# Optimization experiments

Hardware: AMD Instinct MI355X
Metric: run time of the kernel (lower is better)

Reference implementation:

```python
import jax, jax.numpy as jnp
import numpy as np

D_MODEL = 768
N_HEADS = 12
D_HEAD = D_MODEL // N_HEADS
B, S = 2, 2048


def setup_inputs() -> dict:
    key = jax.random.key(0)
    k1, k2, k3, k4, k5 = jax.random.split(key, 5)
    scale_in = 1.0 / np.sqrt(D_MODEL)
    return {
        "x": jax.random.normal(k1, (B, S, D_MODEL), dtype=jnp.float32),
        "W_qkv": jax.random.normal(k2, (3 * D_MODEL, D_MODEL), dtype=jnp.float32) * scale_in,
        "b_qkv": jax.random.normal(k3, (3 * D_MODEL,), dtype=jnp.float32) * 0.01,
        "W_o": jax.random.normal(k4, (D_MODEL, D_MODEL), dtype=jnp.float32) * scale_in,
        "b_o": jax.random.normal(k5, (D_MODEL,), dtype=jnp.float32) * 0.01,
    }


def reference(x, W_qkv, b_qkv, W_o, b_o):
    b, s, d = x.shape
    # QKV projection (torch Linear: x @ W^T + b), then split into q, k, v
    qkv = x @ W_qkv.T + b_qkv                      # [b, s, 3d]
    q, k, v = jnp.split(qkv, 3, axis=-1)           # each [b, s, d]
    # reshape to heads: [b, h, s, d_head]
    def to_heads(t):
        return t.reshape(b, s, N_HEADS, D_HEAD).transpose(0, 2, 1, 3)
    q, k, v = to_heads(q), to_heads(k), to_heads(v)
    # full attention scores with causal mask
    scores = jnp.einsum("bhqd,bhkd->bhqk", q, k) * (D_HEAD ** -0.5)
    causal = jnp.tril(jnp.ones((s, s), dtype=bool))
    scores = jnp.where(causal, scores, -jnp.inf)
    probas = jax.nn.softmax(scores, axis=-1)
    z = jnp.einsum("bhqk,bhkd->bhqd", probas, v)   # [b, h, s, d_head]
    z = z.transpose(0, 2, 1, 3).reshape(b, s, d)
    return z @ W_o.T + b_o
```

## Files before the change

### kernel.cpp

```cpp
#include <hip/hip_runtime.h>
#include <hip/hip_bf16.h>
#include <stdint.h>

#define D_MODEL 768
#define N_HEADS 12
#define D_HEAD  64
#define BATCH   2
#define SEQ     2048
#define M_TOTAL (BATCH*SEQ)
#define N_QKV   (3*D_MODEL)

typedef float  floatx4 __attribute__((ext_vector_type(4)));
typedef short  shortx8 __attribute__((ext_vector_type(8)));

#if __has_builtin(__builtin_amdgcn_exp2f)
#define EXP2(x) __builtin_amdgcn_exp2f(x)
#else
#define EXP2(x) exp2f(x)
#endif

#define Q_SCALE 0.18033688011112042f

static __device__ __forceinline__ unsigned short f2bf(float f) {
  __hip_bfloat16 h = __float2bfloat16(f);
  return *reinterpret_cast<unsigned short*>(&h);
}

static __device__ __forceinline__ void gload_lds16(const void* g, void* l) {
  auto gp = reinterpret_cast<const uint32_t __attribute__((address_space(1)))*>(
      reinterpret_cast<uintptr_t>(g));
  auto lp = reinterpret_cast<uint32_t __attribute__((address_space(3)))*>(
      reinterpret_cast<uintptr_t>(l));
  __builtin_amdgcn_global_load_lds(gp, lp, 16, 0, 0);
}

__global__ void convert_bf16_kernel(const float* __restrict__ x,
                                    const float* __restrict__ wqkv,
                                    const float* __restrict__ wo,
                                    unsigned short* __restrict__ xb,
                                    unsigned short* __restrict__ wqkvb,
                                    unsigned short* __restrict__ wob) {
  const int NX = M_TOTAL * D_MODEL / 4;
  const int NW = N_QKV * D_MODEL / 4;
  const int NO = D_MODEL * D_MODEL / 4;
  const int total = NX + NW + NO;
  for (int i = blockIdx.x * blockDim.x + threadIdx.x; i < total;
       i += gridDim.x * blockDim.x) {
    const float4* src; unsigned short* dst; int j;
    if (i < NX)            { src = (const float4*)x;    dst = xb;    j = i; }
    else if (i < NX + NW)  { src = (const float4*)wqkv; dst = wqkvb; j = i - NX; }
    else                   { src = (const float4*)wo;   dst = wob;   j = i - NX - NW; }
    float4 v = src[j];
    ushort4 o;
    o.x = f2bf(v.x); o.y = f2bf(v.y); o.z = f2bf(v.z); o.w = f2bf(v.w);
    *(ushort4*)(dst + (size_t)j * 4) = o;
  }
}

__launch_bounds__(256, 3)
__global__ void qkv_gemm_kernel(const unsigned short* __restrict__ Xb,
                                const unsigned short* __restrict__ Wb,
                                const float* __restrict__ bias,
                                unsigned short* __restrict__ Qb,
                                unsigned short* __restrict__ Kb,
                                unsigned short* __restrict__ Vt) {
  __shared__ unsigned short Asub[128 * 32];
  __shared__ unsigned short Bsub[128 * 32];
  const int tid  = threadIdx.x;
  const int wave = tid >> 6;
  const int lane = tid & 63;
  const int flat = blockIdx.x;
  const int swz  = (flat & 7) * 72 + (flat >> 3);
  const int m0 = (swz / 18) * 128;
  const int n0 = (swz % 18) * 128;
  const int wm = (wave >> 1) * 64;
  const int wn = (wave & 1) * 64;
  const int srow = lane >> 2;
  const int scol = (lane & 3) * 8;
  const int col  = lane & 15;
  const int grp  = lane >> 4;
  floatx4 acc[4][4] = {};
  for (int kt = 0; kt < D_MODEL; kt += 32) {
    #pragma unroll
    for (int i = 0; i < 2; ++i) {
      int c = wave * 2 + i;
      int row = c * 16 + srow;
      gload_lds16(Xb + (size_t)(m0 + row) * D_MODEL + kt + scol, &Asub[c * 512]);
      gload_lds16(Wb + (size_t)(n0 + row) * D_MODEL + kt + scol, &Bsub[c * 512]);
    }
    __syncthreads();
    shortx8 af[4], bf[4];
    #pragma unroll
    for (int t = 0; t < 4; ++t) {
      af[t] = *(const shortx8*)&Asub[(wm + t * 16 + col) * 32 + grp * 8];
      bf[t] = *(const shortx8*)&Bsub[(wn + t * 16 + col) * 32 + grp * 8];
    }
    #pragma unroll
    for (int i = 0; i < 4; ++i)
      #pragma unroll
      for (int j = 0; j < 4; ++j)
        acc[i][j] = __builtin_amdgcn_mfma_f32_16x16x32_bf16(af[i], bf[j], acc[i][j], 0, 0, 0);
    __syncthreads();
  }
  #pragma unroll
  for (int i = 0; i < 4; ++i) {
    int mbase = m0 + wm + i * 16 + grp * 4;
    int b = mbase >> 11;
    int s = mbase & 2047;
    #pragma unroll
    for (int j = 0; j < 4; ++j) {
      int n   = n0 + wn + j * 16 + col;
      int sel = n / D_MODEL;
      int c   = n % D_MODEL;
      int h   = c >> 6, d = c & 63;
      int bh  = b * N_HEADS + h;
      float bv = bias[n];
      if (sel == 0) {
        #pragma unroll
        for (int r = 0; r < 4; ++r)
          Qb[((size_t)bh * SEQ + s + r) * D_HEAD + d] = f2bf((acc[i][j][r] + bv) * Q_SCALE);
      } else if (sel == 1) {
        #pragma unroll
        for (int r = 0; r < 4; ++r)
          Kb[((size_t)bh * SEQ + s + r) * D_HEAD + d] = f2bf(acc[i][j][r] + bv);
      } else {
        ushort4 o;
        o.x = f2bf(acc[i][j][0] + bv);
        o.y = f2bf(acc[i][j][1] + bv);
        o.z = f2bf(acc[i][j][2] + bv);
        o.w = f2bf(acc[i][j][3] + bv);
        *(ushort4*)&Vt[((size_t)bh * D_HEAD + d) * SEQ + s] = o;
      }
    }
  }
}

__launch_bounds__(256, 3)
__global__ void attn_kernel(const unsigned short* __restrict__ Qb,
                            const unsigned short* __restrict__ Kb,
                            const unsigned short* __restrict__ Vt,
                            unsigned short* __restrict__ Zb) {
  __shared__ unsigned short K_lds[2][64 * 64];
  __shared__ unsigned short V_lds[2][64 * 64];
  __shared__ unsigned short pw[4][16 * 136];
  const int tid  = threadIdx.x;
  const int w    = tid >> 6;
  const int lane = tid & 63;
  const int col  = lane & 15;
  const int grp  = lane >> 4;

  const int i  = blockIdx.x;
  const int v  = (i & 7) * 96 + (i >> 3);
  const int bh = v >> 5;
  const int qb = 31 - (v & 31);
  const int q0 = qb * 64;
  const int qgb = q0 + w * 16;
  const int ntiles = qb + 1;

  const unsigned short* Qrow = Qb + ((size_t)bh * SEQ + qgb + col) * D_HEAD;
  const shortx8 qf0 = *(const shortx8*)(Qrow + grp * 8);
  const shortx8 qf1 = *(const shortx8*)(Qrow + 32 + grp * 8);

  const size_t kbase = (size_t)bh * SEQ * D_HEAD;
  const size_t vbase = (size_t)bh * D_HEAD * SEQ;

  floatx4 acc[4] = {};
  float mrun = -1e30f, lrun = 0.f;
  unsigned short* pwv = pw[w];

#define STAGE(buf, kv0) do {                                                   \
    const size_t kg = kbase + (size_t)(kv0) * D_HEAD;                          \
    _Pragma("unroll")                                                          \
    for (int s_ = 0; s_ < 2; ++s_) {                                           \
      int L_ = w * 2048 + s_ * 1024 + lane * 16;                               \
      int g_ = L_ ^ (((L_ >> 7) & 7) << 4);                                    \
      gload_lds16(Kb + kg + (g_ >> 1), &K_lds[buf][w * 1024 + s_ * 512]);      \
      int row_ = g_ >> 7, cb_ = g_ & 127;                                      \
      gload_lds16(Vt + vbase + (size_t)row_ * SEQ + (kv0) + (cb_ >> 1),        \
                  &V_lds[buf][w * 1024 + s_ * 512]);                           \
    }                                                                          \
  } while (0)

  STAGE(0, 0);
  __syncthreads();

  for (int t = 0; t < ntiles; ++t) {
    const int cur = t & 1;
    const int kv0 = t * 64;
    if (t + 1 < ntiles) STAGE(cur ^ 1, (t + 1) * 64);

    floatx4 st[4];
    #pragma unroll
    for (int nt = 0; nt < 4; ++nt) {
      int r0 = (nt * 16 + col) * 64;
      int sw = (col & 7) << 3;
      shortx8 kf0 = *(const shortx8*)&K_lds[cur][(r0 + grp * 8) ^ sw];
      shortx8 kf1 = *(const shortx8*)&K_lds[cur][(r0 + 32 + grp * 8) ^ sw];
      floatx4 s = {};
      s = __builtin_amdgcn_mfma_f32_16x16x32_bf16(kf0, qf0, s, 0, 0, 0);
      s = __builtin_amdgcn_mfma_f32_16x16x32_bf16(kf1, qf1, s, 0, 0, 0);
      st[nt] = s;
    }
    float tmax = -1e30f;
    if (t == ntiles - 1) {
      const int q = qgb + col;
      #pragma unroll
      for (int nt = 0; nt < 4; ++nt)
        #pragma unroll
        for (int r = 0; r < 4; ++r) {
          int kv = kv0 + nt * 16 + grp * 4 + r;
          float sv = (kv <= q) ? st[nt][r] : -1e30f;
          st[nt][r] = sv;
          tmax = fmaxf(tmax, sv);
        }
    } else {
      #pragma unroll
      for (int nt = 0; nt < 4; ++nt)
        #pragma unroll
        for (int r = 0; r < 4; ++r) tmax = fmaxf(tmax, st[nt][r]);
    }
    tmax = fmaxf(tmax, __shfl_xor(tmax, 16));
    tmax = fmaxf(tmax, __shfl_xor(tmax, 32));
    const float mnew  = fmaxf(mrun, tmax);
    const float alpha = EXP2(mrun - mnew);
    mrun = mnew;
    float rs = 0.f;
    #pragma unroll
    for (int nt = 0; nt < 4; ++nt)
      #pragma unroll
      for (int r = 0; r < 4; ++r) {
        float pv = EXP2(st[nt][r] - mnew);
        st[nt][r] = pv;
        rs += pv;
      }
    rs += __shfl_xor(rs, 16);
    rs += __shfl_xor(rs, 32);
    lrun = lrun * alpha + rs;
    #pragma unroll
    for (int r = 0; r < 4; ++r) {
      float ar = __shfl(alpha, grp * 4 + r);
      #pragma unroll
      for (int dn = 0; dn < 4; ++dn) acc[dn][r] *= ar;
    }
    #pragma unroll
    for (int nt = 0; nt < 4; ++nt) {
      ushort4 po;
      po.x = f2bf(st[nt][0]); po.y = f2bf(st[nt][1]);
      po.z = f2bf(st[nt][2]); po.w = f2bf(st[nt][3]);
      *(ushort4*)&pwv[col * 136 + nt * 16 + grp * 4] = po;
    }
    #pragma unroll
    for (int m = 0; m < 2; ++m) {
      shortx8 pf = *(const shortx8*)&pwv[col * 136 + m * 32 + grp * 8];
      #pragma unroll
      for (int dn = 0; dn < 4; ++dn) {
        int vr = (dn * 16 + col) * 64;
        shortx8 vf = *(const shortx8*)&V_lds[cur][(vr + m * 32 + grp * 8) ^ ((col & 7) << 3)];
        acc[dn] = __builtin_amdgcn_mfma_f32_16x16x32_bf16(pf, vf, acc[dn], 0, 0, 0);
      }
    }
    __syncthreads();
  }
#undef STAGE

  const int b = bh / N_HEADS, h = bh % N_HEADS;
  #pragma unroll
  for (int r = 0; r < 4; ++r) {
    float lr = __shfl(lrun, grp * 4 + r);
    float li = 1.0f / lr;
    int q = qgb + grp * 4 + r;
    #pragma unroll
    for (int dn = 0; dn < 4; ++dn)
      Zb[((size_t)b * SEQ + q) * D_MODEL + h * 64 + dn * 16 + col] = f2bf(acc[dn][r] * li);
  }
}

__launch_bounds__(256, 4)
__global__ void out_gemm_kernel(const unsigned short* __restrict__ Zb,
                                const unsigned short* __restrict__ Wob,
                                const float* __restrict__ bo,
                                float* __restrict__ Out) {
  __shared__ unsigned short Asub[128 * 32];
  __shared__ unsigned short Bsub[64 * 32];
  const int tid  = threadIdx.x;
  const int wave = tid >> 6;
  const int lane = tid & 63;
  const int flat = blockIdx.x;
  const int swz  = (flat & 7) * 48 + (flat >> 3);
  const int m0 = (swz / 12) * 128;
  const int n0 = (swz % 12) * 64;
  const int wm = (wave >> 1) * 64;
  const int wn = (wave & 1) * 32;
  const int srow = lane >> 2;
  const int scol = (lane & 3) * 8;
  const int col  = lane & 15;
  const int grp  = lane >> 4;
  floatx4 acc[4][2] = {};
  for (int kt = 0; kt < D_MODEL; kt += 32) {
    #pragma unroll
    for (int i = 0; i < 2; ++i) {
      int g = wave * 2 + i;
      gload_lds16(Zb + (size_t)(m0 + g * 16 + srow) * D_MODEL + kt + scol, &Asub[g * 512]);
    }
    gload_lds16(Wob + (size_t)(n0 + wave * 16 + srow) * D_MODEL + kt + scol, &Bsub[wave * 512]);
    __syncthreads();
    shortx8 af[4], bf[2];
    #pragma unroll
    for (int t = 0; t < 4; ++t)
      af[t] = *(const shortx8*)&Asub[(wm + t * 16 + col) * 32 + grp * 8];
    #pragma unroll
    for (int u = 0; u < 2; ++u)
      bf[u] = *(const shortx8*)&Bsub[(wn + u * 16 + col) * 32 + grp * 8];
    #pragma unroll
    for (int i = 0; i < 4; ++i)
      #pragma unroll
      for (int jj = 0; jj < 2; ++jj)
        acc[i][jj] = __builtin_amdgcn_mfma_f32_16x16x32_bf16(af[i], bf[jj], acc[i][jj], 0, 0, 0);
    __syncthreads();
  }
  #pragma unroll
  for (int i = 0; i < 4; ++i) {
    int mbase = m0 + wm + i * 16 + grp * 4;
    #pragma unroll
    for (int jj = 0; jj < 2; ++jj) {
      int n = n0 + wn + jj * 16 + col;
      float bv = bo[n];
      #pragma unroll
      for (int r = 0; r < 4; ++r)
        Out[(size_t)(mbase + r) * D_MODEL + n] = acc[i][jj][r] + bv;
    }
  }
}

extern "C" void kernel_launch(void* const* d_in, const int* in_sizes, int n_in,
                              void* d_out, int out_size, void* d_ws, size_t ws_size,
                              hipStream_t stream) {
  const float* x    = (const float*)d_in[0];
  const float* Wqkv = (const float*)d_in[1];
  const float* bqkv = (const float*)d_in[2];
  const float* Wo   = (const float*)d_in[3];
  const float* bo   = (const float*)d_in[4];
  float* out = (float*)d_out;

  unsigned short* ws = (unsigned short*)d_ws;
  const size_t SZ_X   = (size_t)M_TOTAL * D_MODEL;
  const size_t SZ_WQ  = (size_t)N_QKV * D_MODEL;
  const size_t SZ_WO  = (size_t)D_MODEL * D_MODEL;
  unsigned short* Xb    = ws;
  unsigned short* Wqkvb = Xb + SZ_X;
  unsigned short* Wob   = Wqkvb + SZ_WQ;
  unsigned short* Qb    = Wob + SZ_WO;
  unsigned short* Kb    = Qb + SZ_X;
  unsigned short* Vt    = Kb + SZ_X;
  unsigned short* Zb    = Vt + SZ_X;

  convert_bf16_kernel<<<dim3(1024), dim3(256), 0, stream>>>(x, Wqkv, Wo, Xb, Wqkvb, Wob);
  qkv_gemm_kernel<<<dim3(8 * 72), dim3(256), 0, stream>>>(
      Xb, Wqkvb, bqkv, Qb, Kb, Vt);
  attn_kernel<<<dim3(8 * 96), dim3(256), 0, stream>>>(Qb, Kb, Vt, Zb);
  out_gemm_kernel<<<dim3(8 * 48), dim3(256), 0, stream>>>(
      Zb, Wob, bo, out);
}
```

Measured before the change: 170.5 us.

## Double-buffer GEMM LDS tiles and pair causal query blocks in attention

Both GEMM kernels now use double-buffered LDS tiles. The next K-slice is prefetched while MFMAs run on the current one, and only one barrier is needed per iteration. The attention kernel launches half as many blocks, and each block handles a short query tile (p) and its complementary long one (31-p). This evens out the causal work per block, so the tail of imbalanced blocks should shrink. The cost is doubled LDS in the GEMMs, which could lower occupancy. With only 384 attention blocks there may also be too little parallelism to fill the CUs.

```diff
diff --git a/kernel.cpp b/kernel.cpp
--- a/kernel.cpp
+++ b/kernel.cpp
@@ -64,8 +64,8 @@
                                 unsigned short* __restrict__ Qb,
                                 unsigned short* __restrict__ Kb,
                                 unsigned short* __restrict__ Vt) {
-  __shared__ unsigned short Asub[128 * 32];
-  __shared__ unsigned short Bsub[128 * 32];
+  __shared__ unsigned short Asub[2][128 * 32];
+  __shared__ unsigned short Bsub[2][128 * 32];
   const int tid  = threadIdx.x;
   const int wave = tid >> 6;
   const int lane = tid & 63;
@@ -80,20 +80,29 @@
   const int col  = lane & 15;
   const int grp  = lane >> 4;
   floatx4 acc[4][4] = {};
+
+#define QSTAGE(buf, kt) do {                                                     \
+    _Pragma("unroll")                                                            \
+    for (int i_ = 0; i_ < 2; ++i_) {                                             \
+      int c_ = wave * 2 + i_;                                                    \
+      int row_ = c_ * 16 + srow;                                                 \
+      gload_lds16(Xb + (size_t)(m0 + row_) * D_MODEL + (kt) + scol,              \
+                  &Asub[buf][c_ * 512]);                                         \
+      gload_lds16(Wb + (size_t)(n0 + row_) * D_MODEL + (kt) + scol,              \
+                  &Bsub[buf][c_ * 512]);                                         \
+    }                                                                            \
+  } while (0)
+
+  QSTAGE(0, 0);
+  __syncthreads();
   for (int kt = 0; kt < D_MODEL; kt += 32) {
-    #pragma unroll
-    for (int i = 0; i < 2; ++i) {
-      int c = wave * 2 + i;
-      int row = c * 16 + srow;
-      gload_lds16(Xb + (size_t)(m0 + row) * D_MODEL + kt + scol, &Asub[c * 512]);
-      gload_lds16(Wb + (size_t)(n0 + row) * D_MODEL + kt + scol, &Bsub[c * 512]);
-    }
-    __syncthreads();
+    const int cur = (kt >> 5) & 1;
+    if (kt + 32 < D_MODEL) QSTAGE(cur ^ 1, kt + 32);
     shortx8 af[4], bf[4];
     #pragma unroll
     for (int t = 0; t < 4; ++t) {
-      af[t] = *(const shortx8*)&Asub[(wm + t * 16 + col) * 32 + grp * 8];
-      bf[t] = *(const shortx8*)&Bsub[(wn + t * 16 + col) * 32 + grp * 8];
+      af[t] = *(const shortx8*)&Asub[cur][(wm + t * 16 + col) * 32 + grp * 8];
+      bf[t] = *(const shortx8*)&Bsub[cur][(wn + t * 16 + col) * 32 + grp * 8];
     }
     #pragma unroll
     for (int i = 0; i < 4; ++i)
@@ -102,6 +111,8 @@
         acc[i][j] = __builtin_amdgcn_mfma_f32_16x16x32_bf16(af[i], bf[j], acc[i][j], 0, 0, 0);
     __syncthreads();
   }
+#undef QSTAGE
+
   #pragma unroll
   for (int i = 0; i < 4; ++i) {
     int mbase = m0 + wm + i * 16 + grp * 4;
@@ -150,22 +161,13 @@
   const int grp  = lane >> 4;
 
   const int i  = blockIdx.x;
-  const int v  = (i & 7) * 96 + (i >> 3);
-  const int bh = v >> 5;
-  const int qb = 31 - (v & 31);
-  const int q0 = qb * 64;
-  const int qgb = q0 + w * 16;
-  const int ntiles = qb + 1;
-
-  const unsigned short* Qrow = Qb + ((size_t)bh * SEQ + qgb + col) * D_HEAD;
-  const shortx8 qf0 = *(const shortx8*)(Qrow + grp * 8);
-  const shortx8 qf1 = *(const shortx8*)(Qrow + 32 + grp * 8);
+  const int u  = (i & 7) * 48 + (i >> 3);
+  const int bh = u >> 4;
+  const int p  = u & 15;
 
   const size_t kbase = (size_t)bh * SEQ * D_HEAD;
   const size_t vbase = (size_t)bh * D_HEAD * SEQ;
-
-  floatx4 acc[4] = {};
-  float mrun = -1e30f, lrun = 0.f;
+  const int b = bh / N_HEADS, h = bh % N_HEADS;
   unsigned short* pwv = pw[w];
 
 #define STAGE(buf, kv0) do {                                                   \
@@ -181,98 +183,111 @@
     }                                                                          \
   } while (0)
 
-  STAGE(0, 0);
-  __syncthreads();
-
-  for (int t = 0; t < ntiles; ++t) {
-    const int cur = t & 1;
-    const int kv0 = t * 64;
-    if (t + 1 < ntiles) STAGE(cur ^ 1, (t + 1) * 64);
-
-    floatx4 st[4];
-    #pragma unroll
-    for (int nt = 0; nt < 4; ++nt) {
-      int r0 = (nt * 16 + col) * 64;
-      int sw = (col & 7) << 3;
-      shortx8 kf0 = *(const shortx8*)&K_lds[cur][(r0 + grp * 8) ^ sw];
-      shortx8 kf1 = *(const shortx8*)&K_lds[cur][(r0 + 32 + grp * 8) ^ sw];
-      floatx4 s = {};
-      s = __builtin_amdgcn_mfma_f32_16x16x32_bf16(kf0, qf0, s, 0, 0, 0);
-      s = __builtin_amdgcn_mfma_f32_16x16x32_bf16(kf1, qf1, s, 0, 0, 0);
-      st[nt] = s;
-    }
-    float tmax = -1e30f;
-    if (t == ntiles - 1) {
-      const int q = qgb + col;
+  for (int pass = 0; pass < 2; ++pass) {
+    const int qb = pass ? (31 - p) : p;
+    const int q0 = qb * 64;
+    const int qgb = q0 + w * 16;
+    const int ntiles = qb + 1;
+
+    const unsigned short* Qrow = Qb + ((size_t)bh * SEQ + qgb + col) * D_HEAD;
+    const shortx8 qf0 = *(const shortx8*)(Qrow + grp * 8);
+    const shortx8 qf1 = *(const shortx8*)(Qrow + 32 + grp * 8);
+
+    floatx4 acc[4] = {};
+    float mrun = -1e30f, lrun = 0.f;
+
+    STAGE(0, 0);
+    __syncthreads();
+
+    for (int t = 0; t < ntiles; ++t) {
+      const int cur = t & 1;
+      const int kv0 = t * 64;
+      if (t + 1 < ntiles) STAGE(cur ^ 1, (t + 1) * 64);
+
+      floatx4 st[4];
+      #pragma unroll
+      for (int nt = 0; nt < 4; ++nt) {
+        int r0 = (nt * 16 + col) * 64;
+        int sw = (col & 7) << 3;
+        shortx8 kf0 = *(const shortx8*)&K_lds[cur][(r0 + grp * 8) ^ sw];
+        shortx8 kf1 = *(const shortx8*)&K_lds[cur][(r0 + 32 + grp * 8) ^ sw];
+        floatx4 s = {};
+        s = __builtin_amdgcn_mfma_f32_16x16x32_bf16(kf0, qf0, s, 0, 0, 0);
+        s = __builtin_amdgcn_mfma_f32_16x16x32_bf16(kf1, qf1, s, 0, 0, 0);
+        st[nt] = s;
+      }
+      float tmax = -1e30f;
+      if (t == ntiles - 1) {
+        const int q = qgb + col;
+        #pragma unroll
+        for (int nt = 0; nt < 4; ++nt)
+          #pragma unroll
+          for (int r = 0; r < 4; ++r) {
+            int kv = kv0 + nt * 16 + grp * 4 + r;
+            float sv = (kv <= q) ? st[nt][r] : -1e30f;
+            st[nt][r] = sv;
+            tmax = fmaxf(tmax, sv);
+          }
+      } else {
+        #pragma unroll
+        for (int nt = 0; nt < 4; ++nt)
+          #pragma unroll
+          for (int r = 0; r < 4; ++r) tmax = fmaxf(tmax, st[nt][r]);
+      }
+      tmax = fmaxf(tmax, __shfl_xor(tmax, 16));
+      tmax = fmaxf(tmax, __shfl_xor(tmax, 32));
+      const float mnew  = fmaxf(mrun, tmax);
+      const float alpha = EXP2(mrun - mnew);
+      mrun = mnew;
+      float rs = 0.f;
       #pragma unroll
       for (int nt = 0; nt < 4; ++nt)
         #pragma unroll
         for (int r = 0; r < 4; ++r) {
-          int kv = kv0 + nt * 16 + grp * 4 + r;
-          float sv = (kv <= q) ? st[nt][r] : -1e30f;
-          st[nt][r] = sv;
-          tmax = fmaxf(tmax, sv);
+          float pv = EXP2(st[nt][r] - mnew);
+          st[nt][r] = pv;
+          rs += pv;
         }
-    } else {
-      #pragma unroll
-      for (int nt = 0; nt < 4; ++nt)
-        #pragma unroll
-        for (int r = 0; r < 4; ++r) tmax = fmaxf(tmax, st[nt][r]);
-    }
-    tmax = fmaxf(tmax, __shfl_xor(tmax, 16));
-    tmax = fmaxf(tmax, __shfl_xor(tmax, 32));
-    const float mnew  = fmaxf(mrun, tmax);
-    const float alpha = EXP2(mrun - mnew);
-    mrun = mnew;
-    float rs = 0.f;
-    #pragma unroll
-    for (int nt = 0; nt < 4; ++nt)
+      rs += __shfl_xor(rs, 16);
+      rs += __shfl_xor(rs, 32);
+      lrun = lrun * alpha + rs;
       #pragma unroll
       for (int r = 0; r < 4; ++r) {
-        float pv = EXP2(st[nt][r] - mnew);
-        st[nt][r] = pv;
-        rs += pv;
-      }
-    rs += __shfl_xor(rs, 16);
-    rs += __shfl_xor(rs, 32);
-    lrun = lrun * alpha + rs;
+        float ar = __shfl(alpha, grp * 4 + r);
+        #pragma unroll
+        for (int dn = 0; dn < 4; ++dn) acc[dn][r] *= ar;
+      }
+      #pragma unroll
+      for (int nt = 0; nt < 4; ++nt) {
+        ushort4 po;
+        po.x = f2bf(st[nt][0]); po.y = f2bf(st[nt][1]);
+        po.z = f2bf(st[nt][2]); po.w = f2bf(st[nt][3]);
+        *(ushort4*)&pwv[col * 136 + nt * 16 + grp * 4] = po;
+      }
+      #pragma unroll
+      for (int m = 0; m < 2; ++m) {
+        shortx8 pf = *(const shortx8*)&pwv[col * 136 + m * 32 + grp * 8];
+        #pragma unroll
+        for (int dn = 0; dn < 4; ++dn) {
+          int vr = (dn * 16 + col) * 64;
+          shortx8 vf = *(const shortx8*)&V_lds[cur][(vr + m * 32 + grp * 8) ^ ((col & 7) << 3)];
+          acc[dn] = __builtin_amdgcn_mfma_f32_16x16x32_bf16(pf, vf, acc[dn], 0, 0, 0);
+        }
+      }
+      __syncthreads();
+    }
+
     #pragma unroll
     for (int r = 0; r < 4; ++r) {
-      float ar = __shfl(alpha, grp * 4 + r);
-      #pragma unroll
-      for (int dn = 0; dn < 4; ++dn) acc[dn][r] *= ar;
-    }
-    #pragma unroll
-    for (int nt = 0; nt < 4; ++nt) {
-      ushort4 po;
-      po.x = f2bf(st[nt][0]); po.y = f2bf(st[nt][1]);
-      po.z = f2bf(st[nt][2]); po.w = f2bf(st[nt][3]);
-      *(ushort4*)&pwv[col * 136 + nt * 16 + grp * 4] = po;
-    }
-    #pragma unroll
-    for (int m = 0; m < 2; ++m) {
-      shortx8 pf = *(const shortx8*)&pwv[col * 136 + m * 32 + grp * 8];
-      #pragma unroll
-      for (int dn = 0; dn < 4; ++dn) {
-        int vr = (dn * 16 + col) * 64;
-        shortx8 vf = *(const shortx8*)&V_lds[cur][(vr + m * 32 + grp * 8) ^ ((col & 7) << 3)];
-        acc[dn] = __builtin_amdgcn_mfma_f32_16x16x32_bf16(pf, vf, acc[dn], 0, 0, 0);
-      }
-    }
-    __syncthreads();
+      float lr = __shfl(lrun, grp * 4 + r);
+      float li = 1.0f / lr;
+      int q = qgb + grp * 4 + r;
+      #pragma unroll
+      for (int dn = 0; dn < 4; ++dn)
+        Zb[((size_t)b * SEQ + q) * D_MODEL + h * 64 + dn * 16 + col] = f2bf(acc[dn][r] * li);
+    }
   }
 #undef STAGE
-
-  const int b = bh / N_HEADS, h = bh % N_HEADS;
-  #pragma unroll
-  for (int r = 0; r < 4; ++r) {
-    float lr = __shfl(lrun, grp * 4 + r);
-    float li = 1.0f / lr;
-    int q = qgb + grp * 4 + r;
-    #pragma unroll
-    for (int dn = 0; dn < 4; ++dn)
-      Zb[((size_t)b * SEQ + q) * D_MODEL + h * 64 + dn * 16 + col] = f2bf(acc[dn][r] * li);
-  }
 }
 
 __launch_bounds__(256, 4)
@@ -280,8 +295,8 @@
                                 const unsigned short* __restrict__ Wob,
                                 const float* __restrict__ bo,
                                 float* __restrict__ Out) {
-  __shared__ unsigned short Asub[128 * 32];
-  __shared__ unsigned short Bsub[64 * 32];
+  __shared__ unsigned short Asub[2][128 * 32];
+  __shared__ unsigned short Bsub[2][64 * 32];
   const int tid  = threadIdx.x;
   const int wave = tid >> 6;
   const int lane = tid & 63;
@@ -296,21 +311,30 @@
   const int col  = lane & 15;
   const int grp  = lane >> 4;
   floatx4 acc[4][2] = {};
+
+#define OSTAGE(buf, kt) do {                                                     \
+    _Pragma("unroll")                                                            \
+    for (int i_ = 0; i_ < 2; ++i_) {                                             \
+      int g_ = wave * 2 + i_;                                                    \
+      gload_lds16(Zb + (size_t)(m0 + g_ * 16 + srow) * D_MODEL + (kt) + scol,    \
+                  &Asub[buf][g_ * 512]);                                         \
+    }                                                                            \
+    gload_lds16(Wob + (size_t)(n0 + wave * 16 + srow) * D_MODEL + (kt) + scol,   \
+                &Bsub[buf][wave * 512]);                                         \
+  } while (0)
+
+  OSTAGE(0, 0);
+  __syncthreads();
   for (int kt = 0; kt < D_MODEL; kt += 32) {
-    #pragma unroll
-    for (int i = 0; i < 2; ++i) {
-      int g = wave * 2 + i;
-      gload_lds16(Zb + (size_t)(m0 + g * 16 + srow) * D_MODEL + kt + scol, &Asub[g * 512]);
-    }
-    gload_lds16(Wob + (size_t)(n0 + wave * 16 + srow) * D_MODEL + kt + scol, &Bsub[wave * 512]);
-    __syncthreads();
+    const int cur = (kt >> 5) & 1;
+    if (kt + 32 < D_MODEL) OSTAGE(cur ^ 1, kt + 32);
     shortx8 af[4], bf[2];
     #pragma unroll
     for (int t = 0; t < 4; ++t)
-      af[t] = *(const shortx8*)&Asub[(wm + t * 16 + col) * 32 + grp * 8];
+      af[t] = *(const shortx8*)&Asub[cur][(wm + t * 16 + col) * 32 + grp * 8];
     #pragma unroll
     for (int u = 0; u < 2; ++u)
-      bf[u] = *(const shortx8*)&Bsub[(wn + u * 16 + col) * 32 + grp * 8];
+      bf[u] = *(const shortx8*)&Bsub[cur][(wn + u * 16 + col) * 32 + grp * 8];
     #pragma unroll
     for (int i = 0; i < 4; ++i)
       #pragma unroll
@@ -318,6 +342,8 @@
         acc[i][jj] = __builtin_amdgcn_mfma_f32_16x16x32_bf16(af[i], bf[jj], acc[i][jj], 0, 0, 0);
     __syncthreads();
   }
+#undef OSTAGE
+
   #pragma unroll
   for (int i = 0; i < 4; ++i) {
     int mbase = m0 + wm + i * 16 + grp * 4;
@@ -357,7 +383,7 @@
   convert_bf16_kernel<<<dim3(1024), dim3(256), 0, stream>>>(x, Wqkv, Wo, Xb, Wqkvb, Wob);
   qkv_gemm_kernel<<<dim3(8 * 72), dim3(256), 0, stream>>>(
       Xb, Wqkvb, bqkv, Qb, Kb, Vt);
-  attn_kernel<<<dim3(8 * 96), dim3(256), 0, stream>>>(Qb, Kb, Vt, Zb);
+  attn_kernel<<<dim3(8 * 48), dim3(256), 0, stream>>>(Qb, Kb, Vt, Zb);
   out_gemm_kernel<<<dim3(8 * 48), dim3(256), 0, stream>>>(
       Zb, Wob, bo, out);
 }
```

New measurement: 153.6 us. -9.9%, faster.
